# Kernel optimization log

Hardware: AMD Instinct MI355X
Metric: run time of the kernel (lower is better)

The kernel has to match this reference:

```python
import jax, jax.numpy as jnp
import numpy as np

N, E, P = 50000, 1600000, 500000
IN_DIM, HID, OUT = 512, 128, 64
EPS = 1e-5


def setup_inputs() -> dict:
    key = jax.random.key(0)
    ks = jax.random.split(key, 16)
    d = {}
    d['x'] = jax.random.normal(ks[0], (N, IN_DIM), dtype=jnp.float32)
    d['ei'] = jax.random.randint(ks[1], (2, E), 0, N, dtype=jnp.int32)
    d['src'] = jax.random.randint(ks[2], (P,), 0, N, dtype=jnp.int32)
    d['dst'] = jax.random.randint(ks[3], (P,), 0, N, dtype=jnp.int32)
    # GCNConv layer 1 params
    d['W1'] = jax.random.normal(ks[4], (IN_DIM, HID), dtype=jnp.float32) / np.sqrt(IN_DIM)
    d['b1'] = jnp.zeros((HID,), jnp.float32)
    d['bn1_gamma'] = jnp.ones((HID,), jnp.float32)
    d['bn1_beta'] = jnp.zeros((HID,), jnp.float32)
    d['bn1_mean'] = jnp.zeros((HID,), jnp.float32)
    d['bn1_var'] = jnp.ones((HID,), jnp.float32)
    # GCNConv layer 2 params
    d['W2'] = jax.random.normal(ks[5], (HID, OUT), dtype=jnp.float32) / np.sqrt(HID)
    d['b2'] = jnp.zeros((OUT,), jnp.float32)
    d['bn2_gamma'] = jnp.ones((OUT,), jnp.float32)
    d['bn2_beta'] = jnp.zeros((OUT,), jnp.float32)
    d['bn2_mean'] = jnp.zeros((OUT,), jnp.float32)
    d['bn2_var'] = jnp.ones((OUT,), jnp.float32)
    # edge head MLP
    d['hW1'] = jax.random.normal(ks[6], (2 * OUT, OUT), dtype=jnp.float32) / np.sqrt(2 * OUT)
    d['hb1'] = jnp.zeros((OUT,), jnp.float32)
    d['hW2'] = jax.random.normal(ks[7], (OUT, 1), dtype=jnp.float32) / np.sqrt(OUT)
    d['hb2'] = jnp.zeros((1,), jnp.float32)
    return d


def gcn_conv(x, ei, W, b):
    """PyG-style GCNConv: add self-loops, symmetric deg^-1/2 normalization."""
    xw = x @ W  # [N, F]
    row, col = ei[0], ei[1]
    ones = jnp.ones((ei.shape[1],), x.dtype)
    deg = jax.ops.segment_sum(ones, col, num_segments=N) + 1.0  # +1 for self-loop
    dinv = jax.lax.rsqrt(deg)
    norm = dinv[row] * dinv[col]  # [E]
    agg = jax.ops.segment_sum(norm[:, None] * xw[row], col, num_segments=N)
    # self-loop contribution: dinv[i]^2 * xw[i]
    return agg + (dinv * dinv)[:, None] * xw + b


def bn_eval(x, gamma, beta, mean, var):
    return (x - mean) * jax.lax.rsqrt(var + EPS) * gamma + beta


def reference(x, ei, src, dst, W1, b1, bn1_gamma, bn1_beta, bn1_mean, bn1_var,
              W2, b2, bn2_gamma, bn2_beta, bn2_mean, bn2_var, hW1, hb1, hW2, hb2):
    h = jax.nn.relu(bn_eval(gcn_conv(x, ei, W1, b1), bn1_gamma, bn1_beta, bn1_mean, bn1_var))
    # dropout is identity in eval mode
    z = jax.nn.relu(bn_eval(gcn_conv(h, ei, W2, b2), bn2_gamma, bn2_beta, bn2_mean, bn2_var))
    pair = jnp.concatenate([z[src], z[dst]], axis=1)  # [P, 2*OUT]
    hmid = jax.nn.relu(pair @ hW1 + hb1)
    logits = hmid @ hW2 + hb2  # [P, 1]
    return jax.nn.sigmoid(logits).squeeze(-1)
```

## Files before the change

### kernel.cpp

```cpp
#include <hip/hip_runtime.h>
#include <math.h>


typedef __attribute__((ext_vector_type(8))) short short8x;
typedef __attribute__((ext_vector_type(8))) _Float16 half8x;
typedef __attribute__((ext_vector_type(4))) float f32x4;

__device__ __forceinline__ unsigned short f2bf(float f) {
  unsigned int u = __float_as_uint(f);
  unsigned int r = u + 0x7FFFu + ((u >> 16) & 1u);
  return (unsigned short)(r >> 16);
}
__device__ __forceinline__ unsigned short f2h(float f) {
  union { _Float16 h; unsigned short u; } cv;
  cv.h = (_Float16)f;
  return cv.u;
}


__global__ void zero_int_kernel(int* __restrict__ p, int n) {
  int i = blockIdx.x * blockDim.x + threadIdx.x;
  if (i < n) p[i] = 0;
}

__global__ __launch_bounds__(256) void binA_hist_kernel(const int* __restrict__ col,
                                                        int* __restrict__ bucket_count, int E,
                                                        int NBK) {
  __shared__ int hist[256];
  const int tid = threadIdx.x;
  hist[tid] = 0;
  __syncthreads();
  const int base = blockIdx.x * 4096;
#pragma unroll
  for (int j = 0; j < 16; ++j) {
    int i = base + j * 256 + tid;
    if (i < E) atomicAdd(&hist[((unsigned int)col[i]) >> 8], 1);
  }
  __syncthreads();
  if (tid < NBK) {
    int h = hist[tid];
    if (h) atomicAdd(&bucket_count[tid], h);
  }
}

__global__ __launch_bounds__(256) void scan_buckets_kernel(const int* __restrict__ bucket_count,
                                                           int* __restrict__ bucket_start,
                                                           int* __restrict__ bcur,
                                                           int* __restrict__ offs_n, int NBK,
                                                           int E) {
  __shared__ int ws[4];
  const int tid = threadIdx.x;
  const int lane = tid & 63;
  const int wid = tid >> 6;
  int v = (tid < NBK) ? bucket_count[tid] : 0;
  int incl = v;
#pragma unroll
  for (int d = 1; d < 64; d <<= 1) {
    int t = __shfl_up(incl, d, 64);
    if (lane >= d) incl += t;
  }
  if (lane == 63) ws[wid] = incl;
  __syncthreads();
  int woff = 0;
#pragma unroll
  for (int w = 0; w < 4; ++w)
    if (w < wid) woff += ws[w];
  int excl = woff + incl - v;
  if (tid < NBK) {
    bucket_start[tid] = excl;
    bcur[tid] = excl;
  }
  if (tid == 0) {
    bucket_start[NBK] = E;
    *offs_n = E;
  }
}

__global__ __launch_bounds__(256) void binA_scatter_kernel(const int* __restrict__ row,
                                                           const int* __restrict__ col,
                                                           int* __restrict__ bcur,
                                                           unsigned int* __restrict__ staging,
                                                           int E, int NBK) {
  __shared__ int hist[256];
  const int tid = threadIdx.x;
  hist[tid] = 0;
  __syncthreads();
  const int base = blockIdx.x * 4096;
  unsigned int payload[16];
  int bk[16];
#pragma unroll
  for (int j = 0; j < 16; ++j) {
    int i = base + j * 256 + tid;
    if (i < E) {
      unsigned int c = (unsigned int)__builtin_nontemporal_load(&col[i]);
      unsigned int r = (unsigned int)__builtin_nontemporal_load(&row[i]);
      payload[j] = (c << 16) | r;
      bk[j] = (int)(c >> 8);
      atomicAdd(&hist[bk[j]], 1);
    } else {
      bk[j] = -1;
    }
  }
  __syncthreads();
  if (tid < NBK) {
    int h = hist[tid];
    hist[tid] = h ? atomicAdd(&bcur[tid], h) : 0;
  }
  __syncthreads();
#pragma unroll
  for (int j = 0; j < 16; ++j) {
    if (bk[j] >= 0) {
      int p = atomicAdd(&hist[bk[j]], 1);
      staging[p] = payload[j];
    }
  }
}

__global__ __launch_bounds__(256) void binB1_kernel(const unsigned int* __restrict__ staging,
                                                    const int* __restrict__ bucket_start,
                                                    int* __restrict__ offs,
                                                    float* __restrict__ dinv, int N) {
  __shared__ int cnt[256];
  __shared__ int ws[4];
  const int b = blockIdx.x;
  const int n0 = b * 256;
  const int tid = threadIdx.x;
  cnt[tid] = 0;
  __syncthreads();
  const int s = bucket_start[b];
  const int e = bucket_start[b + 1];
  for (int t = s + tid; t < e; t += 256) {
    atomicAdd(&cnt[(staging[t] >> 16) & 255u], 1);
  }
  __syncthreads();
  const int deg = cnt[tid];
  const int lane = tid & 63;
  const int wid = tid >> 6;
  int incl = deg;
#pragma unroll
  for (int d = 1; d < 64; d <<= 1) {
    int t = __shfl_up(incl, d, 64);
    if (lane >= d) incl += t;
  }
  if (lane == 63) ws[wid] = incl;
  __syncthreads();
  int woff = 0;
#pragma unroll
  for (int w = 0; w < 4; ++w)
    if (w < wid) woff += ws[w];
  const int excl = woff + incl - deg;
  const int node = n0 + tid;
  if (node < N) {
    offs[node] = s + excl;
    dinv[node] = rsqrtf((float)deg + 1.0f);
  }
}

__global__ __launch_bounds__(512) void binB2_kernel(const unsigned int* __restrict__ staging,
                                                    const int* __restrict__ offs,
                                                    const int* __restrict__ bucket_start,
                                                    const float* __restrict__ dinv,
                                                    unsigned int* __restrict__ csr, int N) {
  __shared__ int cur[256];
  const int b = blockIdx.x;
  const int n0 = b * 256;
  const int tid = threadIdx.x;
  if (tid < 256 && n0 + tid < N) cur[tid] = offs[n0 + tid];
  __syncthreads();
  const int s = bucket_start[b];
  const int e = bucket_start[b + 1];
  for (int t = s + tid; t < e; t += 512) {
    unsigned int v = __builtin_nontemporal_load(&staging[t]);
    int cl = (int)((v >> 16) & 255u);
    unsigned int r = v & 0xFFFFu;
    unsigned int wd = f2bf(dinv[r]);
    int p = atomicAdd(&cur[cl], 1);
    csr[p] = (wd << 16) | r;
  }
}

__global__ __launch_bounds__(256) void prep_all_kernel(const float* __restrict__ W1,
                                                       const float* __restrict__ W2,
                                                       const float* __restrict__ hW1,
                                                       unsigned short* __restrict__ bfW1,
                                                       unsigned short* __restrict__ bfW2,
                                                       unsigned short* __restrict__ bfH) {
  int idx = blockIdx.x * blockDim.x + threadIdx.x;
  const float* W;
  unsigned short* out;
  int K, N, base, mode;
  if (idx < 8192) {
    W = W1; out = bfW1; K = 512; N = 128; base = 0; mode = 0;
  } else if (idx < 9216) {
    W = W2; out = bfW2; K = 128; N = 64; base = 8192; mode = 0;
  } else if (idx < 10240) {
    W = hW1; out = bfH; K = 64; N = 128; base = 9216; mode = 1;
  } else {
    return;
  }
  int id = idx - base;
  int lane = id & 63;
  int t = id >> 6;
  int KS = K / 32;
  int ks = t % KS;
  int nt = t / KS;
  int n = nt * 16 + (lane & 15);
  int k0 = ks * 32 + (lane >> 4) * 8;
  unsigned short* o = out + (size_t)id * 8;
#pragma unroll
  for (int j = 0; j < 8; ++j) {
    int k = k0 + j;
    float v;
    if (mode == 0)
      v = W[(size_t)k * N + n];
    else
      v = (n < 64) ? W[(size_t)k * 64 + n] : W[(size_t)(64 + k) * 64 + (n - 64)];
    o[j] = f2bf(v);
  }
}

template <int K, int N, bool ABF16, bool OUTF16>
__global__ __launch_bounds__(256) void mfma_gemm_kernel(const void* __restrict__ Ap,
                                                        const unsigned short* __restrict__ Bfrag,
                                                        unsigned short* __restrict__ Cout, int M) {
  constexpr int KS = K / 32;
  constexpr int NT = N / 16;
  const int lane = threadIdx.x & 63;
  const int wid = threadIdx.x >> 6;
  const int quad = lane >> 4;
  const int lc = lane & 15;
  const int mbase = blockIdx.x * 128 + wid * 32;
  if (mbase >= M) return;

  f32x4 acc[2][NT];
#pragma unroll
  for (int mt = 0; mt < 2; ++mt)
#pragma unroll
    for (int nt = 0; nt < NT; ++nt) acc[mt][nt] = (f32x4){0.f, 0.f, 0.f, 0.f};

  int r0 = mbase + lc;
  int r1 = mbase + 16 + lc;
  if (r0 >= M) r0 = M - 1;
  if (r1 >= M) r1 = M - 1;

#pragma unroll
  for (int ks = 0; ks < KS; ++ks) {
    const int k0 = ks * 32 + quad * 8;
    short8x a[2];
    if constexpr (ABF16) {
      const unsigned short* A = (const unsigned short*)Ap;
      a[0] = *(const short8x*)(A + (size_t)r0 * K + k0);
      a[1] = *(const short8x*)(A + (size_t)r1 * K + k0);
    } else {
      const float* A = (const float*)Ap;
      const float4* p0 = (const float4*)(A + (size_t)r0 * K + k0);
      const float4* p1 = (const float4*)(A + (size_t)r1 * K + k0);
      float4 u0 = p0[0], v0 = p0[1];
      float4 u1 = p1[0], v1 = p1[1];
      short8x t0, t1;
      t0[0] = (short)f2bf(u0.x); t0[1] = (short)f2bf(u0.y);
      t0[2] = (short)f2bf(u0.z); t0[3] = (short)f2bf(u0.w);
      t0[4] = (short)f2bf(v0.x); t0[5] = (short)f2bf(v0.y);
      t0[6] = (short)f2bf(v0.z); t0[7] = (short)f2bf(v0.w);
      t1[0] = (short)f2bf(u1.x); t1[1] = (short)f2bf(u1.y);
      t1[2] = (short)f2bf(u1.z); t1[3] = (short)f2bf(u1.w);
      t1[4] = (short)f2bf(v1.x); t1[5] = (short)f2bf(v1.y);
      t1[6] = (short)f2bf(v1.z); t1[7] = (short)f2bf(v1.w);
      a[0] = t0;
      a[1] = t1;
    }
#pragma unroll
    for (int nt = 0; nt < NT; ++nt) {
      short8x b = *(const short8x*)(Bfrag + (((size_t)nt * KS + ks) * 64 + lane) * 8);
      acc[0][nt] = __builtin_amdgcn_mfma_f32_16x16x32_bf16(a[0], b, acc[0][nt], 0, 0, 0);
      acc[1][nt] = __builtin_amdgcn_mfma_f32_16x16x32_bf16(a[1], b, acc[1][nt], 0, 0, 0);
    }
  }

#pragma unroll
  for (int mt = 0; mt < 2; ++mt)
#pragma unroll
    for (int nt = 0; nt < NT; ++nt)
#pragma unroll
      for (int reg = 0; reg < 4; ++reg) {
        int row = mbase + mt * 16 + quad * 4 + reg;
        if (row < M) {
          float v = acc[mt][nt][reg];
          Cout[(size_t)row * N + nt * 16 + lc] = OUTF16 ? f2h(v) : f2bf(v);
        }
      }
}

template <int F>
__global__ __launch_bounds__(256) void agg_fast_kernel(
    const unsigned short* __restrict__ xw, const int* __restrict__ offs,
    const unsigned int* __restrict__ csr, const float* __restrict__ dinv,
    const float* __restrict__ bias, const float* __restrict__ gamma,
    const float* __restrict__ beta, const float* __restrict__ mean,
    const float* __restrict__ var, unsigned short* __restrict__ out, int N) {
  constexpr int G = F / 2;
  constexpr int NPB = 256 / G;
  const int li = threadIdx.x % G;
  const int i = blockIdx.x * NPB + threadIdx.x / G;
  if (i >= N) return;
  const unsigned int* xw32 = (const unsigned int*)xw;
  const float di = dinv[i];
  const int s = offs[i], e = offs[i + 1];
  float accL = 0.f, accH = 0.f;
  int t = s;
  for (; t + 16 <= e; t += 16) {
    unsigned int ent[16];
#pragma unroll
    for (int j = 0; j < 16; ++j) ent[j] = __builtin_nontemporal_load(&csr[t + j]);
    unsigned int gv[16];
#pragma unroll
    for (int j = 0; j < 16; ++j) gv[j] = xw32[(size_t)(ent[j] & 0xFFFFu) * G + li];
#pragma unroll
    for (int j = 0; j < 16; ++j) {
      float w = __uint_as_float(ent[j] & 0xFFFF0000u);
      accL += w * __uint_as_float(gv[j] << 16);
      accH += w * __uint_as_float(gv[j] & 0xFFFF0000u);
    }
  }
  for (; t + 4 <= e; t += 4) {
    unsigned int ent[4];
#pragma unroll
    for (int j = 0; j < 4; ++j) ent[j] = __builtin_nontemporal_load(&csr[t + j]);
    unsigned int gv[4];
#pragma unroll
    for (int j = 0; j < 4; ++j) gv[j] = xw32[(size_t)(ent[j] & 0xFFFFu) * G + li];
#pragma unroll
    for (int j = 0; j < 4; ++j) {
      float w = __uint_as_float(ent[j] & 0xFFFF0000u);
      accL += w * __uint_as_float(gv[j] << 16);
      accH += w * __uint_as_float(gv[j] & 0xFFFF0000u);
    }
  }
  for (; t < e; ++t) {
    unsigned int ee = __builtin_nontemporal_load(&csr[t]);
    unsigned int gv = xw32[(size_t)(ee & 0xFFFFu) * G + li];
    float w = __uint_as_float(ee & 0xFFFF0000u);
    accL += w * __uint_as_float(gv << 16);
    accH += w * __uint_as_float(gv & 0xFFFF0000u);
  }
  const int f0 = 2 * li, f1 = f0 + 1;
  unsigned int sv = xw32[(size_t)i * G + li];
  float v0 = di * accL + di * di * __uint_as_float(sv << 16) + bias[f0];
  float v1 = di * accH + di * di * __uint_as_float(sv & 0xFFFF0000u) + bias[f1];
  v0 = (v0 - mean[f0]) * rsqrtf(var[f0] + 1e-5f) * gamma[f0] + beta[f0];
  v1 = (v1 - mean[f1]) * rsqrtf(var[f1] + 1e-5f) * gamma[f1] + beta[f1];
  unsigned int packed =
      (unsigned int)f2bf(fmaxf(v0, 0.f)) | ((unsigned int)f2bf(fmaxf(v1, 0.f)) << 16);
  ((unsigned int*)out)[(size_t)i * G + li] = packed;
}

__global__ __launch_bounds__(256) void head2_kernel(
    const unsigned short* __restrict__ zh, const int* __restrict__ src,
    const int* __restrict__ dst, const float* __restrict__ hb1,
    const float* __restrict__ hw2, const float* __restrict__ hb2,
    float* __restrict__ out, int P) {
  const int lane = threadIdx.x & 63;
  const int lc = lane & 15;
  const int quad = lane >> 4;
  float b1v[16], w2v[16];
#pragma unroll
  for (int t = 0; t < 16; ++t) {
    b1v[t] = hb1[quad * 16 + t];
    w2v[t] = hw2[quad * 16 + t];
  }
  const float bias2 = hb2[0];
  const int nchunks = (P + 15) / 16;
  const int gw = blockIdx.x * 4 + (threadIdx.x >> 6);
  const int nw = gridDim.x * 4;

  for (int ch = gw; ch < nchunks; ch += nw) {
    int p = ch * 16 + lc;
    int pc = p < P ? p : P - 1;
    int s = __builtin_nontemporal_load(&src[pc]);
    int d = __builtin_nontemporal_load(&dst[pc]);
    const half8x* pa = (const half8x*)(zh + (size_t)s * 128 + quad * 16);
    const half8x* pb = (const half8x*)(zh + (size_t)d * 128 + 64 + quad * 16);
    half8x a0 = pa[0], a1 = pa[1];
    half8x b0 = pb[0], b1 = pb[1];
    float acc = 0.f;
#pragma unroll
    for (int t = 0; t < 8; ++t) {
      float hm = fmaxf((float)a0[t] + (float)b0[t] + b1v[t], 0.f);
      acc = fmaf(hm, w2v[t], acc);
    }
#pragma unroll
    for (int t = 0; t < 8; ++t) {
      float hm = fmaxf((float)a1[t] + (float)b1[t] + b1v[8 + t], 0.f);
      acc = fmaf(hm, w2v[8 + t], acc);
    }
    acc += __shfl_xor(acc, 16, 64);
    acc += __shfl_xor(acc, 32, 64);
    if (quad == 0 && p < P) {
      float o = 1.0f / (1.0f + __expf(-(acc + bias2)));
      __builtin_nontemporal_store(o, &out[p]);
    }
  }
}


extern "C" void kernel_launch(void* const* d_in, const int* in_sizes, int n_in,
                              void* d_out, int out_size, void* d_ws, size_t ws_size,
                              hipStream_t stream) {
  const float* x = (const float*)d_in[0];
  const int* ei = (const int*)d_in[1];
  const int* src = (const int*)d_in[2];
  const int* dst = (const int*)d_in[3];
  const float* W1 = (const float*)d_in[4];
  const float* b1 = (const float*)d_in[5];
  const float* g1 = (const float*)d_in[6];
  const float* be1 = (const float*)d_in[7];
  const float* mu1 = (const float*)d_in[8];
  const float* va1 = (const float*)d_in[9];
  const float* W2 = (const float*)d_in[10];
  const float* b2 = (const float*)d_in[11];
  const float* g2 = (const float*)d_in[12];
  const float* be2 = (const float*)d_in[13];
  const float* mu2 = (const float*)d_in[14];
  const float* va2 = (const float*)d_in[15];
  const float* hW1 = (const float*)d_in[16];
  const float* hb1 = (const float*)d_in[17];
  const float* hW2 = (const float*)d_in[18];
  const float* hb2 = (const float*)d_in[19];
  float* out = (float*)d_out;

  const int N = in_sizes[0] / 512;
  const int E = in_sizes[1] / 2;
  const int P = in_sizes[2];
  const int* row = ei;
  const int* col = ei + E;
  const int NBK = (N + 255) / 256;
  const int NAB = (E + 4095) / 4096;

  char* wp = (char*)d_ws;
  auto alloc = [&](size_t bytes) {
    char* p = wp;
    wp += (bytes + 255) & ~(size_t)255;
    return p;
  };
  unsigned short* xw1 = (unsigned short*)alloc((size_t)N * 128 * 2);
  unsigned short* h = (unsigned short*)alloc((size_t)N * 128 * 2);
  unsigned short* xw2 = (unsigned short*)alloc((size_t)N * 64 * 2);
  unsigned short* z = (unsigned short*)alloc((size_t)N * 64 * 2);
  unsigned short* zh = (unsigned short*)alloc((size_t)N * 128 * 2);
  float* dinv = (float*)alloc((size_t)N * 4);
  int* offs = (int*)alloc((size_t)(N + 1) * 4);
  unsigned int* csr = (unsigned int*)alloc((size_t)E * 4);
  unsigned int* staging = (unsigned int*)alloc((size_t)E * 4);
  int* bucket_count = (int*)alloc((size_t)NBK * 4);
  int* bucket_start = (int*)alloc((size_t)(NBK + 1) * 4);
  int* bcur = (int*)alloc((size_t)NBK * 4);
  unsigned short* bfW1 = (unsigned short*)alloc(512 * 128 * 2);
  unsigned short* bfW2 = (unsigned short*)alloc(128 * 64 * 2);
  unsigned short* bfH = (unsigned short*)alloc(128 * 64 * 2);
  (void)ws_size;
  (void)n_in;
  (void)out_size;

  hipLaunchKernelGGL(zero_int_kernel, dim3((NBK + 255) / 256), dim3(256), 0, stream, bucket_count,
                     NBK);
  hipLaunchKernelGGL(binA_hist_kernel, dim3(NAB), dim3(256), 0, stream, col, bucket_count, E, NBK);
  hipLaunchKernelGGL(scan_buckets_kernel, dim3(1), dim3(256), 0, stream, bucket_count,
                     bucket_start, bcur, offs + N, NBK, E);
  hipLaunchKernelGGL(binA_scatter_kernel, dim3(NAB), dim3(256), 0, stream, row, col, bcur, staging,
                     E, NBK);
  hipLaunchKernelGGL(binB1_kernel, dim3(NBK), dim3(256), 0, stream, staging, bucket_start, offs,
                     dinv, N);
  hipLaunchKernelGGL(binB2_kernel, dim3(NBK), dim3(512), 0, stream, staging, offs, bucket_start,
                     dinv, csr, N);

  hipLaunchKernelGGL(prep_all_kernel, dim3(40), dim3(256), 0, stream, W1, W2, hW1, bfW1, bfW2,
                     bfH);

  hipLaunchKernelGGL((mfma_gemm_kernel<512, 128, false, false>), dim3((N + 127) / 128), dim3(256),
                     0, stream, x, bfW1, xw1, N);
  hipLaunchKernelGGL((agg_fast_kernel<128>), dim3((N + 3) / 4), dim3(256), 0, stream, xw1, offs,
                     csr, dinv, b1, g1, be1, mu1, va1, h, N);

  hipLaunchKernelGGL((mfma_gemm_kernel<128, 64, true, false>), dim3((N + 127) / 128), dim3(256), 0,
                     stream, h, bfW2, xw2, N);
  hipLaunchKernelGGL((agg_fast_kernel<64>), dim3((N + 7) / 8), dim3(256), 0, stream, xw2, offs,
                     csr, dinv, b2, g2, be2, mu2, va2, z, N);

  hipLaunchKernelGGL((mfma_gemm_kernel<64, 128, true, true>), dim3((N + 127) / 128), dim3(256), 0,
                     stream, z, bfH, zh, N);
  hipLaunchKernelGGL(head2_kernel, dim3(2048), dim3(256), 0, stream, zh, src, dst, hb1, hW2, hb2,
                     out, P);
}
```

Baseline: 402.8 us.

## Split GCN aggregation across feature slices via a second grid dimension

The aggregation kernel now assigns 16 lanes per node, each covering a 32-feature slice, with blockIdx.y selecting the slice. Each node's CSR list is therefore read once per slice. Nontemporal CSR loads become normal loads so the repeated reads can hit cache. The goal is more parallelism, smaller per-node feature gathers, and better L2 locality for the gathered rows, at the cost of redundant CSR traffic and per-edge index work.

```diff
diff --git a/kernel.cpp b/kernel.cpp
--- a/kernel.cpp
+++ b/kernel.cpp
@@ -292,17 +292,19 @@
 }
 
 template <int F>
-__global__ __launch_bounds__(256) void agg_fast_kernel(
+__global__ __launch_bounds__(256) void agg_slice_kernel(
     const unsigned short* __restrict__ xw, const int* __restrict__ offs,
     const unsigned int* __restrict__ csr, const float* __restrict__ dinv,
     const float* __restrict__ bias, const float* __restrict__ gamma,
     const float* __restrict__ beta, const float* __restrict__ mean,
     const float* __restrict__ var, unsigned short* __restrict__ out, int N) {
-  constexpr int G = F / 2;
+  constexpr int RD = F / 2;
+  constexpr int G = 16;
   constexpr int NPB = 256 / G;
-  const int li = threadIdx.x % G;
+  const int li = threadIdx.x & (G - 1);
   const int i = blockIdx.x * NPB + threadIdx.x / G;
   if (i >= N) return;
+  const int fb = blockIdx.y * G;
   const unsigned int* xw32 = (const unsigned int*)xw;
   const float di = dinv[i];
   const int s = offs[i], e = offs[i + 1];
@@ -311,10 +313,10 @@
   for (; t + 16 <= e; t += 16) {
     unsigned int ent[16];
 #pragma unroll
-    for (int j = 0; j < 16; ++j) ent[j] = __builtin_nontemporal_load(&csr[t + j]);
+    for (int j = 0; j < 16; ++j) ent[j] = csr[t + j];
     unsigned int gv[16];
 #pragma unroll
-    for (int j = 0; j < 16; ++j) gv[j] = xw32[(size_t)(ent[j] & 0xFFFFu) * G + li];
+    for (int j = 0; j < 16; ++j) gv[j] = xw32[(size_t)(ent[j] & 0xFFFFu) * RD + fb + li];
 #pragma unroll
     for (int j = 0; j < 16; ++j) {
       float w = __uint_as_float(ent[j] & 0xFFFF0000u);
@@ -325,10 +327,10 @@
   for (; t + 4 <= e; t += 4) {
     unsigned int ent[4];
 #pragma unroll
-    for (int j = 0; j < 4; ++j) ent[j] = __builtin_nontemporal_load(&csr[t + j]);
+    for (int j = 0; j < 4; ++j) ent[j] = csr[t + j];
     unsigned int gv[4];
 #pragma unroll
-    for (int j = 0; j < 4; ++j) gv[j] = xw32[(size_t)(ent[j] & 0xFFFFu) * G + li];
+    for (int j = 0; j < 4; ++j) gv[j] = xw32[(size_t)(ent[j] & 0xFFFFu) * RD + fb + li];
 #pragma unroll
     for (int j = 0; j < 4; ++j) {
       float w = __uint_as_float(ent[j] & 0xFFFF0000u);
@@ -337,21 +339,21 @@
     }
   }
   for (; t < e; ++t) {
-    unsigned int ee = __builtin_nontemporal_load(&csr[t]);
-    unsigned int gv = xw32[(size_t)(ee & 0xFFFFu) * G + li];
+    unsigned int ee = csr[t];
+    unsigned int gv = xw32[(size_t)(ee & 0xFFFFu) * RD + fb + li];
     float w = __uint_as_float(ee & 0xFFFF0000u);
     accL += w * __uint_as_float(gv << 16);
     accH += w * __uint_as_float(gv & 0xFFFF0000u);
   }
-  const int f0 = 2 * li, f1 = f0 + 1;
-  unsigned int sv = xw32[(size_t)i * G + li];
+  const int f0 = 2 * (fb + li), f1 = f0 + 1;
+  unsigned int sv = xw32[(size_t)i * RD + fb + li];
   float v0 = di * accL + di * di * __uint_as_float(sv << 16) + bias[f0];
   float v1 = di * accH + di * di * __uint_as_float(sv & 0xFFFF0000u) + bias[f1];
   v0 = (v0 - mean[f0]) * rsqrtf(var[f0] + 1e-5f) * gamma[f0] + beta[f0];
   v1 = (v1 - mean[f1]) * rsqrtf(var[f1] + 1e-5f) * gamma[f1] + beta[f1];
   unsigned int packed =
       (unsigned int)f2bf(fmaxf(v0, 0.f)) | ((unsigned int)f2bf(fmaxf(v1, 0.f)) << 16);
-  ((unsigned int*)out)[(size_t)i * G + li] = packed;
+  ((unsigned int*)out)[(size_t)i * RD + fb + li] = packed;
 }
 
 __global__ __launch_bounds__(256) void head2_kernel(
@@ -478,13 +480,13 @@
 
   hipLaunchKernelGGL((mfma_gemm_kernel<512, 128, false, false>), dim3((N + 127) / 128), dim3(256),
                      0, stream, x, bfW1, xw1, N);
-  hipLaunchKernelGGL((agg_fast_kernel<128>), dim3((N + 3) / 4), dim3(256), 0, stream, xw1, offs,
-                     csr, dinv, b1, g1, be1, mu1, va1, h, N);
+  hipLaunchKernelGGL((agg_slice_kernel<128>), dim3((N + 15) / 16, 4), dim3(256), 0, stream, xw1,
+                     offs, csr, dinv, b1, g1, be1, mu1, va1, h, N);
 
   hipLaunchKernelGGL((mfma_gemm_kernel<128, 64, true, false>), dim3((N + 127) / 128), dim3(256), 0,
                      stream, h, bfW2, xw2, N);
-  hipLaunchKernelGGL((agg_fast_kernel<64>), dim3((N + 7) / 8), dim3(256), 0, stream, xw2, offs,
-                     csr, dinv, b2, g2, be2, mu2, va2, z, N);
+  hipLaunchKernelGGL((agg_slice_kernel<64>), dim3((N + 15) / 16, 2), dim3(256), 0, stream, xw2,
+                     offs, csr, dinv, b2, g2, be2, mu2, va2, z, N);
 
   hipLaunchKernelGGL((mfma_gemm_kernel<64, 128, true, true>), dim3((N + 127) / 128), dim3(256), 0,
                      stream, z, bfH, zh, N);
```

New measurement: 414.9 us. +3.0%, slower.

## Sort CSR neighbor lists by source-row block within each destination node

Applied to the files above, without the earlier changes.

The CSR fill kernel now counts edges per (source-row block of 1024, destination node) in a 64KB shared histogram, scans it, and scatters edges so each node's neighbor list is grouped by source row range. This aims to improve locality of the later xw[row] gathers in the aggregation kernels. In exchange the bucket's staging data is read twice, block size drops from 512 to 256, and the large shared allocation reduces occupancy of this kernel.

```diff
diff --git a/kernel.cpp b/kernel.cpp
--- a/kernel.cpp
+++ b/kernel.cpp
@@ -156,26 +156,57 @@
   }
 }
 
-__global__ __launch_bounds__(512) void binB2_kernel(const unsigned int* __restrict__ staging,
-                                                    const int* __restrict__ offs,
+__global__ __launch_bounds__(256) void binB2_kernel(const unsigned int* __restrict__ staging,
                                                     const int* __restrict__ bucket_start,
                                                     const float* __restrict__ dinv,
-                                                    unsigned int* __restrict__ csr, int N) {
-  __shared__ int cur[256];
+                                                    unsigned int* __restrict__ csr) {
+  __shared__ int cnt[64 * 256];
+  __shared__ int ws[4];
   const int b = blockIdx.x;
-  const int n0 = b * 256;
   const int tid = threadIdx.x;
-  if (tid < 256 && n0 + tid < N) cur[tid] = offs[n0 + tid];
+  for (int k = tid; k < 64 * 256; k += 256) cnt[k] = 0;
   __syncthreads();
   const int s = bucket_start[b];
   const int e = bucket_start[b + 1];
-  for (int t = s + tid; t < e; t += 512) {
+  for (int t = s + tid; t < e; t += 256) {
+    unsigned int v = __builtin_nontemporal_load(&staging[t]);
+    int cl = (int)((v >> 16) & 255u);
+    int ph = (int)((v & 0xFFFFu) >> 10);
+    atomicAdd(&cnt[ph * 256 + cl], 1);
+  }
+  __syncthreads();
+  int deg = 0;
+#pragma unroll
+  for (int k = 0; k < 64; ++k) deg += cnt[k * 256 + tid];
+  const int lane = tid & 63;
+  const int wid = tid >> 6;
+  int incl = deg;
+#pragma unroll
+  for (int d = 1; d < 64; d <<= 1) {
+    int t = __shfl_up(incl, d, 64);
+    if (lane >= d) incl += t;
+  }
+  if (lane == 63) ws[wid] = incl;
+  __syncthreads();
+  int woff = 0;
+#pragma unroll
+  for (int w = 0; w < 4; ++w)
+    if (w < wid) woff += ws[w];
+  int pos = s + woff + incl - deg;
+#pragma unroll
+  for (int k = 0; k < 64; ++k) {
+    int c = cnt[k * 256 + tid];
+    cnt[k * 256 + tid] = pos;
+    pos += c;
+  }
+  __syncthreads();
+  for (int t = s + tid; t < e; t += 256) {
     unsigned int v = __builtin_nontemporal_load(&staging[t]);
     int cl = (int)((v >> 16) & 255u);
     unsigned int r = v & 0xFFFFu;
-    unsigned int wd = f2bf(dinv[r]);
-    int p = atomicAdd(&cur[cl], 1);
-    csr[p] = (wd << 16) | r;
+    int ph = (int)(r >> 10);
+    int p = atomicAdd(&cnt[ph * 256 + cl], 1);
+    csr[p] = (((unsigned int)f2bf(dinv[r])) << 16) | r;
   }
 }
 
@@ -470,8 +501,8 @@
                      E, NBK);
   hipLaunchKernelGGL(binB1_kernel, dim3(NBK), dim3(256), 0, stream, staging, bucket_start, offs,
                      dinv, N);
-  hipLaunchKernelGGL(binB2_kernel, dim3(NBK), dim3(512), 0, stream, staging, offs, bucket_start,
-                     dinv, csr, N);
+  hipLaunchKernelGGL(binB2_kernel, dim3(NBK), dim3(256), 0, stream, staging, bucket_start, dinv,
+                     csr);
 
   hipLaunchKernelGGL(prep_all_kernel, dim3(40), dim3(256), 0, stream, W1, W2, hW1, bfW1, bfW2,
                      bfH);
```

New measurement: 410.2 us. No clear change (+1.8%).
